# Kernel tuning notes

Hardware: AMD Instinct MI355X
Metric: run time of the kernel (lower is better)

Reference implementation:

```python
import jax, jax.numpy as jnp
import numpy as np

D = 512
H = 8
G = 4          # GroupNorm groups
EPS = 1e-3     # GroupNorm eps


def group_norm(x):
    # x: (b, n, t, d); torch code normalizes per (batch, group) over (n*t, d/G)
    b, n, t, d = x.shape
    xr = x.reshape(b, n * t, G, d // G)
    mu = xr.mean(axis=(1, 3), keepdims=True)
    var = ((xr - mu) ** 2).mean(axis=(1, 3), keepdims=True)
    return ((xr - mu) * jax.lax.rsqrt(var + EPS)).reshape(b, n, t, d)


def setup_inputs() -> dict:
    key = jax.random.key(0)
    ks = jax.random.split(key, 9)
    s = 1.0 / np.sqrt(D)
    inp = {
        "ind": 0,
        "in_f": jax.random.normal(ks[0], (4, 8, 512, D), dtype=jnp.float32),
        "in_f_kv": jax.random.normal(ks[1], (4, 8, 512, D), dtype=jnp.float32),
        "Wq": jax.random.normal(ks[2], (D, D), dtype=jnp.float32) * s,
        "Wk": jax.random.normal(ks[3], (D, D), dtype=jnp.float32) * s,
        "Wv": jax.random.normal(ks[4], (D, D), dtype=jnp.float32) * s,
        "Wz": jax.random.normal(ks[5], (D, D), dtype=jnp.float32) * s,
        "bz": jnp.zeros((D,), dtype=jnp.float32),
        "W1": jax.random.normal(ks[6], (D, D), dtype=jnp.float32) * s,
        "b1": jnp.full((D,), 0.1, dtype=jnp.float32),
        "W2": jax.random.normal(ks[7], (D, D), dtype=jnp.float32) * s,
        "b2": jnp.full((D,), 0.1, dtype=jnp.float32),
    }
    return inp


def reference(ind, in_f, in_f_kv, Wq, Wk, Wv, Wz, bz, W1, b1, W2, b2):
    b, n, t, d = in_f.shape
    hd = d // H
    scale = 1.0 / np.sqrt(hd)

    _in_f = group_norm(in_f)          # LN_1
    _in_f_kv = group_norm(in_f_kv)    # LN_2

    # torch Linear: y = x @ W.T
    q = group_norm(_in_f @ Wq.T)      # LN_3
    k = group_norm(_in_f_kv @ Wk.T)   # LN_4
    v = _in_f_kv @ Wv.T

    q = q.reshape(b, n, t, H, hd)
    k = k.reshape(b, n, -1, H, hd)
    v = v.reshape(b, n, -1, H, hd)

    logits = jnp.einsum('bnqhd,bnkhd->bnhqk', q, k) * scale
    attn_weights = jax.nn.softmax(logits, axis=-1)
    attn_out = jnp.einsum('bnhqk,bnkhd->bnqhd', attn_weights, v).reshape(b, n, t, d)

    in_f_u1 = attn_out @ Wz.T + bz
    in_f_u2 = jax.nn.leaky_relu(_in_f @ W1.T + b1, negative_slope=0.01) @ W2.T + b2

    out_f = in_f + in_f_u1 + in_f_u2
    return (out_f, attn_weights)
```

## Files before the change

### kernel.cpp

```cpp
#include <hip/hip_runtime.h>
#include <math.h>

#define TDIM 512
#define DDIM 512
#define NTROWS 4096
#define MROWS 16384
#define EPSGN 1e-3f

typedef __attribute__((ext_vector_type(8))) short bf16x8;
typedef __attribute__((ext_vector_type(4))) float f32x4;
typedef __attribute__((ext_vector_type(8))) unsigned short us8;
typedef __attribute__((ext_vector_type(4))) unsigned short us4;

__device__ __forceinline__ unsigned short f2b(float f) {
  unsigned int u = __float_as_uint(f);
  return (unsigned short)((u + 0x7fffu + ((u >> 16) & 1u)) >> 16);
}
__device__ __forceinline__ float b2f(unsigned short h) {
  return __uint_as_float(((unsigned int)h) << 16);
}

#define GLOAD16(g, l)                                                                   \
  __builtin_amdgcn_global_load_lds((const __attribute__((address_space(1))) void*)(g),  \
                                   (__attribute__((address_space(3))) void*)(l), 16, 0, 0)

__global__ __launch_bounds__(256) void stats_cvt(const float* __restrict__ x0,
                                                 const float* __restrict__ x1,
                                                 unsigned short* __restrict__ o0,
                                                 unsigned short* __restrict__ o1,
                                                 float* __restrict__ p0,
                                                 float* __restrict__ p1,
                                                 const float* __restrict__ Wz,
                                                 const float* __restrict__ W2,
                                                 unsigned short* __restrict__ w16s) {
  if (blockIdx.y == 2) {
    const int bid = blockIdx.x;
    if (bid >= 256) return;
    const int c = bid * 256 + threadIdx.x;
    const int t = c >> 15;
    const int off = c & 32767;
    const float* s = t ? W2 : Wz;
    unsigned short* d = w16s + (size_t)(16 + t) * 262144;
    const float4 f0 = *(const float4*)(s + (size_t)off * 8);
    const float4 f1 = *(const float4*)(s + (size_t)off * 8 + 4);
    us8 v;
    v[0] = f2b(f0.x); v[1] = f2b(f0.y); v[2] = f2b(f0.z); v[3] = f2b(f0.w);
    v[4] = f2b(f1.x); v[5] = f2b(f1.y); v[6] = f2b(f1.z); v[7] = f2b(f1.w);
    *(us8*)(d + (size_t)off * 8) = v;
    return;
  }
  const float* x = blockIdx.y ? x1 : x0;
  unsigned short* o = blockIdx.y ? o1 : o0;
  float* part = blockIdx.y ? p1 : p0;
  const int blk = blockIdx.x;
  const int batch = blk >> 7;
  const int chunk = blk & 127;
  const size_t base = (size_t)blk * 32 * 512;
  const int tid = threadIdx.x;
  float s = 0.f, sq = 0.f;
#pragma unroll 4
  for (int it = 0; it < 8; ++it) {
    const size_t e = base + (size_t)it * 2048 + (size_t)tid * 8;
    const float4 f0 = *(const float4*)(x + e);
    const float4 f1 = *(const float4*)(x + e + 4);
    us8 v;
    v[0] = f2b(f0.x); v[1] = f2b(f0.y); v[2] = f2b(f0.z); v[3] = f2b(f0.w);
    v[4] = f2b(f1.x); v[5] = f2b(f1.y); v[6] = f2b(f1.z); v[7] = f2b(f1.w);
    *(us8*)(o + e) = v;
    s += f0.x + f0.y + f0.z + f0.w + f1.x + f1.y + f1.z + f1.w;
    sq += f0.x * f0.x + f0.y * f0.y + f0.z * f0.z + f0.w * f0.w +
          f1.x * f1.x + f1.y * f1.y + f1.z * f1.z + f1.w * f1.w;
  }
  const int wave = tid >> 6, lane = tid & 63;
#pragma unroll
  for (int of = 1; of < 16; of <<= 1) { s += __shfl_xor(s, of); sq += __shfl_xor(sq, of); }
  __shared__ float red[4][4][2];
  if ((lane & 15) == 0) { red[wave][lane >> 4][0] = s; red[wave][lane >> 4][1] = sq; }
  __syncthreads();
  if (tid < 4) {
    float S = 0.f, SQ = 0.f;
#pragma unroll
    for (int w = 0; w < 4; ++w) { S += red[w][tid][0]; SQ += red[w][tid][1]; }
    const int idx = (((batch << 2) | tid) << 7) | chunk;
    part[idx * 2] = S;
    part[idx * 2 + 1] = SQ;
  }
}

__global__ __launch_bounds__(256) void wprep(const float* __restrict__ Wq,
                                             const float* __restrict__ Wk,
                                             const float* __restrict__ Wv,
                                             const float* __restrict__ W1,
                                             const float* __restrict__ p0,
                                             const float* __restrict__ p1,
                                             unsigned short* __restrict__ w16s,
                                             float* __restrict__ corr) {
  const int y = blockIdx.y;
  const int w = y >> 2, b = y & 3;
  const float* W = (w == 0) ? Wq : (w == 1) ? Wk : (w == 2) ? Wv : W1;
  const float* part = (w == 0 || w == 3) ? p0 : p1;
  __shared__ float mrs[4][2];
  if (threadIdx.x < 4) {
    const float* p = part + (((b << 2) | threadIdx.x) << 7) * 2;
    float S = 0.f, SQ = 0.f;
    for (int c = 0; c < 128; ++c) { S += p[c * 2]; SQ += p[c * 2 + 1]; }
    const float inv = 1.f / (float)(NTROWS * 128);
    const float mu = S * inv;
    const float var = SQ * inv - mu * mu;
    const float rs = rsqrtf(var + EPSGN);
    mrs[threadIdx.x][0] = rs;
    mrs[threadIdx.x][1] = mu * rs;
  }
  __syncthreads();
  const int wave = threadIdx.x >> 6, lane = threadIdx.x & 63;
  const int n = blockIdx.x * 4 + wave;
  const int k = lane * 8;
  const int g = lane >> 4;
  const float rs = mrs[g][0], murs = mrs[g][1];
  const float4 f0 = *(const float4*)(W + (size_t)n * 512 + k);
  const float4 f1 = *(const float4*)(W + (size_t)n * 512 + k + 4);
  us8 v;
  v[0] = f2b(f0.x * rs); v[1] = f2b(f0.y * rs); v[2] = f2b(f0.z * rs); v[3] = f2b(f0.w * rs);
  v[4] = f2b(f1.x * rs); v[5] = f2b(f1.y * rs); v[6] = f2b(f1.z * rs); v[7] = f2b(f1.w * rs);
  *(us8*)(w16s + (size_t)((w << 2) | b) * 262144 + (size_t)n * 512 + k) = v;
  float t = (f0.x + f0.y + f0.z + f0.w + f1.x + f1.y + f1.z + f1.w) * murs;
#pragma unroll
  for (int of = 1; of < 64; of <<= 1) t += __shfl_xor(t, of);
  if (lane == 0) corr[(((w << 2) | b) << 9) | n] = t;
}

__global__ __launch_bounds__(256) void gemm_all(const unsigned short* __restrict__ a16,
                                                const unsigned short* __restrict__ akv16,
                                                const unsigned short* __restrict__ w16s,
                                                const float* __restrict__ corr,
                                                unsigned short* __restrict__ q16,
                                                unsigned short* __restrict__ h16,
                                                unsigned short* __restrict__ k16,
                                                unsigned short* __restrict__ vTb,
                                                const float* __restrict__ b1,
                                                float* __restrict__ part_q,
                                                float* __restrict__ part_k,
                                                float* __restrict__ sk) {
  __shared__ __align__(16) unsigned short As[128 * 64];
  __shared__ __align__(16) unsigned short Bs[128 * 64];
  __shared__ float red[8];
  const int p = blockIdx.x + (blockIdx.y << 7) + (blockIdx.z << 10);
  const int xc = p & 7, m = p >> 3;
  const int bxi = (xc << 4) | (m & 15);
  const int yi = (m >> 4) & 7;
  const int z = m >> 7;
  const int tid = threadIdx.x;
  const int wave = tid >> 6, lane = tid & 63;
  const int bm = bxi << 7;
  const int batch = bxi >> 5;
  const bool first = yi < 4;
  const int widx = z ? (first ? 1 : 2) : (first ? 0 : 3);
  const unsigned short* A = z ? akv16 : a16;
  const unsigned short* B = w16s + (size_t)262144 * ((widx << 2) | batch);
  const int bnl = (yi & 3) << 7;
  const int wr = (wave >> 1) << 6;
  const int wc = (wave & 1) << 6;
  const int lr = lane & 15, lg = lane >> 4;

  f32x4 acc[4][4] = {};
  const int srow = lane >> 3;
  const int sslot = (lane & 7) ^ srow;

  for (int k0 = 0; k0 < 512; k0 += 64) {
    __syncthreads();
#pragma unroll
    for (int i = 0; i < 4; ++i) {
      const int ci = wave * 4 + i;
      const int row = ci * 8 + srow;
      GLOAD16(A + (size_t)(bm + row) * 512 + k0 + sslot * 8, (char*)As + ci * 1024);
      GLOAD16(B + (size_t)(bnl + row) * 512 + k0 + sslot * 8, (char*)Bs + ci * 1024);
    }
    __syncthreads();
#pragma unroll
    for (int kk = 0; kk < 64; kk += 32) {
      bf16x8 af[4], bfr[4];
#pragma unroll
      for (int i = 0; i < 4; ++i) {
        const int row = wr + i * 16 + lr;
        af[i] = *(const bf16x8*)&As[row * 64 + ((((kk >> 3) + lg) ^ (row & 7)) << 3)];
      }
#pragma unroll
      for (int j = 0; j < 4; ++j) {
        const int row = wc + j * 16 + lr;
        bfr[j] = *(const bf16x8*)&Bs[row * 64 + ((((kk >> 3) + lg) ^ (row & 7)) << 3)];
      }
#pragma unroll
      for (int i = 0; i < 4; ++i)
#pragma unroll
        for (int j = 0; j < 4; ++j)
          acc[i][j] = __builtin_amdgcn_mfma_f32_16x16x32_bf16(af[i], bfr[j], acc[i][j], 0, 0, 0);
    }
  }

  {
    const float* cb = corr + (((widx << 2) | batch) << 9);
    float cj[4];
#pragma unroll
    for (int j = 0; j < 4; ++j) cj[j] = cb[bnl + wc + j * 16 + lr];
#pragma unroll
    for (int i = 0; i < 4; ++i)
#pragma unroll
      for (int j = 0; j < 4; ++j)
#pragma unroll
        for (int r = 0; r < 4; ++r) acc[i][j][r] -= cj[j];
  }

  if (first) {
    unsigned short* C0 = z ? k16 : q16;
#pragma unroll
    for (int i = 0; i < 4; ++i) {
      const int row0 = bm + wr + i * 16 + lg * 4;
#pragma unroll
      for (int j = 0; j < 4; ++j) {
        const int col = bnl + wc + j * 16 + lr;
#pragma unroll
        for (int r = 0; r < 4; ++r)
          C0[(size_t)(row0 + r) * 512 + col] = f2b(acc[i][j][r]);
      }
    }
    float s = 0.f, sq = 0.f;
#pragma unroll
    for (int i = 0; i < 4; ++i)
#pragma unroll
      for (int j = 0; j < 4; ++j)
#pragma unroll
        for (int r = 0; r < 4; ++r) { const float v = acc[i][j][r]; s += v; sq += v * v; }
#pragma unroll
    for (int o = 32; o > 0; o >>= 1) { s += __shfl_xor(s, o); sq += __shfl_xor(sq, o); }
    if (lane == 0) { red[wave * 2] = s; red[wave * 2 + 1] = sq; }
    __syncthreads();
    if (tid == 0) {
      float* part = z ? part_k : part_q;
      const float S = red[0] + red[2] + red[4] + red[6];
      const float SQ = red[1] + red[3] + red[5] + red[7];
      const int slot = bxi & 31, g = yi;
      const int idx = ((((batch << 2) | g) << 5) | slot) << 1;
      part[idx] = S;
      part[idx + 1] = SQ;
    }
    if (z) {
      const int head = (bnl >> 6) + (wave & 1);
#pragma unroll
      for (int i = 0; i < 4; ++i) {
#pragma unroll
        for (int r = 0; r < 4; ++r) {
          float t = acc[i][0][r] + acc[i][1][r] + acc[i][2][r] + acc[i][3][r];
#pragma unroll
          for (int o = 1; o < 16; o <<= 1) t += __shfl_xor(t, o);
          if (lr == 0)
            sk[(size_t)(bm + wr + i * 16 + lg * 4 + r) * 8 + head] = t;
        }
      }
    }
  } else if (z == 0) {
#pragma unroll
    for (int i = 0; i < 4; ++i) {
      const int row0 = bm + wr + i * 16 + lg * 4;
#pragma unroll
      for (int j = 0; j < 4; ++j) {
        const int col = bnl + wc + j * 16 + lr;
        const float bb = b1[col];
#pragma unroll
        for (int r = 0; r < 4; ++r) {
          float v = acc[i][j][r] + bb;
          v = v > 0.f ? v : 0.01f * v;
          h16[(size_t)(row0 + r) * 512 + col] = f2b(v);
        }
      }
    }
  } else {
#pragma unroll
    for (int i = 0; i < 4; ++i) {
      const int row0 = bm + wr + i * 16 + lg * 4;
#pragma unroll
      for (int j = 0; j < 4; ++j) {
        const int col = bnl + wc + j * 16 + lr;
        us4 pk;
#pragma unroll
        for (int r = 0; r < 4; ++r) pk[r] = f2b(acc[i][j][r]);
        *(us4*)&vTb[((size_t)(row0 >> 9) * 512 + col) * 512 + (row0 & 511)] = pk;
      }
    }
  }
}

__global__ __launch_bounds__(256) void gemm_final(const unsigned short* __restrict__ A0,
                                                  const unsigned short* __restrict__ A1,
                                                  const unsigned short* __restrict__ B0,
                                                  const unsigned short* __restrict__ B1,
                                                  float* __restrict__ Cf,
                                                  const float* __restrict__ bias0,
                                                  const float* __restrict__ bias1,
                                                  const unsigned short* __restrict__ init16) {
  __shared__ __align__(16) unsigned short As[128 * 64];
  __shared__ __align__(16) unsigned short Bs[128 * 64];
  const int p = blockIdx.x + (blockIdx.y << 7);
  const int xc = p & 7, m = p >> 3;
  const int bxi = (xc << 4) | (m & 15);
  const int bni = (m >> 4) & 3;
  const int tid = threadIdx.x;
  const int wave = tid >> 6, lane = tid & 63;
  const int bm = bxi << 7, bn = bni << 7;
  const int wr = (wave >> 1) << 6;
  const int wc = (wave & 1) << 6;
  const int lr = lane & 15, lg = lane >> 4;

  f32x4 acc[4][4] = {};
  const int srow = lane >> 3;
  const int sslot = (lane & 7) ^ srow;

  for (int k0 = 0; k0 < 1024; k0 += 64) {
    const unsigned short* Ab = (k0 < 512) ? A0 : A1;
    const unsigned short* Bb = (k0 < 512) ? B0 : B1;
    const int kl = k0 & 511;
    __syncthreads();
#pragma unroll
    for (int i = 0; i < 4; ++i) {
      const int ci = wave * 4 + i;
      const int row = ci * 8 + srow;
      GLOAD16(Ab + (size_t)(bm + row) * 512 + kl + sslot * 8, (char*)As + ci * 1024);
      GLOAD16(Bb + (size_t)(bn + row) * 512 + kl + sslot * 8, (char*)Bs + ci * 1024);
    }
    __syncthreads();
#pragma unroll
    for (int kk = 0; kk < 64; kk += 32) {
      bf16x8 af[4], bfr[4];
#pragma unroll
      for (int i = 0; i < 4; ++i) {
        const int row = wr + i * 16 + lr;
        af[i] = *(const bf16x8*)&As[row * 64 + ((((kk >> 3) + lg) ^ (row & 7)) << 3)];
      }
#pragma unroll
      for (int j = 0; j < 4; ++j) {
        const int row = wc + j * 16 + lr;
        bfr[j] = *(const bf16x8*)&Bs[row * 64 + ((((kk >> 3) + lg) ^ (row & 7)) << 3)];
      }
#pragma unroll
      for (int i = 0; i < 4; ++i)
#pragma unroll
        for (int j = 0; j < 4; ++j)
          acc[i][j] = __builtin_amdgcn_mfma_f32_16x16x32_bf16(af[i], bfr[j], acc[i][j], 0, 0, 0);
    }
  }

#pragma unroll
  for (int i = 0; i < 4; ++i) {
    const int row0 = bm + wr + i * 16 + lg * 4;
#pragma unroll
    for (int j = 0; j < 4; ++j) {
      const int col = bn + wc + j * 16 + lr;
      const float bb = bias0[col] + bias1[col];
#pragma unroll
      for (int r = 0; r < 4; ++r) {
        const size_t o = (size_t)(row0 + r) * 512 + col;
        Cf[o] = acc[i][j][r] + bb + b2f(init16[o]);
      }
    }
  }
}

__global__ __launch_bounds__(256) void attn_fused(const unsigned short* __restrict__ q16,
                                                  const unsigned short* __restrict__ k16,
                                                  const unsigned short* __restrict__ vT,
                                                  const float* __restrict__ part_q,
                                                  const float* __restrict__ part_k,
                                                  const float* __restrict__ sk,
                                                  float* __restrict__ aw,
                                                  unsigned short* __restrict__ ao16) {
  __shared__ __align__(16) char smem[73728];
  unsigned short* Qs = (unsigned short*)smem;
  unsigned short* Ks = (unsigned short*)(smem + 8192);
  unsigned short* Ps = (unsigned short*)(smem + 40960);
  float* Pf = (float*)smem;
  __shared__ float WM[4][64];
  __shared__ float WS[4][64];
  __shared__ float sk_lds[512];
  __shared__ float cst[2];

  const int p = blockIdx.x;
  const int xcd = p & 7, seq = p >> 3;
  const int bid = (xcd << 5) | (seq >> 3);
  const int q0 = (seq & 7) << 6;
  const int h = bid & 7;
  const int b = bid >> 6;
  const int tid = threadIdx.x;
  const int w = tid >> 6, lane = tid & 63;
  const int lr = lane & 15, lg = lane >> 4;
  const int srow = lane >> 3;
  const int sslot = (lane & 7) ^ srow;

  const size_t hb = (size_t)(bid >> 3) * (512 * 512);
  const unsigned short* Qg = q16 + hb + h * 64;
  const unsigned short* Kg = k16 + hb + h * 64;
  const unsigned short* Vg = vT + hb + (size_t)h * 64 * 512;

  if (tid == 0) {
    const int pbase = (((b << 2) | (h >> 1)) << 6);
    const float* pq = part_q + pbase;
    const float* pk = part_k + pbase;
    float Sq = 0.f, SQq = 0.f, Sk = 0.f, SQk = 0.f;
    for (int c = 0; c < 32; ++c) {
      Sq += pq[c * 2]; SQq += pq[c * 2 + 1];
      Sk += pk[c * 2]; SQk += pk[c * 2 + 1];
    }
    const float inv = 1.f / (float)(NTROWS * 128);
    const float muq = Sq * inv, vq = SQq * inv - muq * muq;
    const float muk = Sk * inv, vk = SQk * inv - muk * muk;
    const float a = rsqrtf(vq + EPSGN) * rsqrtf(vk + EPSGN) * 0.125f;
    cst[0] = a;
    cst[1] = a * muq;
  }
  {
    const float* skg = sk + (size_t)(bid >> 3) * 512 * 8 + h;
    for (int j = tid; j < 512; j += 256) sk_lds[j] = skg[(size_t)j * 8];
  }

#pragma unroll
  for (int it = 0; it < 2; ++it) {
    const int ci = w * 2 + it;
    const int row = ci * 8 + srow;
    GLOAD16(Qg + (size_t)(q0 + row) * 512 + sslot * 8, (char*)Qs + ci * 1024);
  }

  f32x4 sc[4][8] = {};

#pragma unroll
  for (int half = 0; half < 2; ++half) {
    __syncthreads();
#pragma unroll
    for (int it = 0; it < 8; ++it) {
      const int ci = w * 8 + it;
      const int row = ci * 8 + srow;
      GLOAD16(Kg + (size_t)(half * 256 + row) * 512 + sslot * 8, (char*)Ks + ci * 1024);
    }
    __syncthreads();
#pragma unroll
    for (int kk = 0; kk < 64; kk += 32) {
      bf16x8 aq[4];
#pragma unroll
      for (int qf = 0; qf < 4; ++qf) {
        const int row = qf * 16 + lr;
        aq[qf] = *(const bf16x8*)&Qs[row * 64 + ((((kk >> 3) + lg) ^ (row & 7)) << 3)];
      }
#pragma unroll
      for (int kf = 0; kf < 4; ++kf) {
        const int row = w * 64 + kf * 16 + lr;
        const bf16x8 bk = *(const bf16x8*)&Ks[row * 64 + ((((kk >> 3) + lg) ^ (row & 7)) << 3)];
#pragma unroll
        for (int qf = 0; qf < 4; ++qf)
          sc[qf][half * 4 + kf] =
              __builtin_amdgcn_mfma_f32_16x16x32_bf16(aq[qf], bk, sc[qf][half * 4 + kf], 0, 0, 0);
      }
    }
  }

  const float aSc = cst[0], cmu = cst[1];
#pragma unroll
  for (int qf = 0; qf < 4; ++qf)
#pragma unroll
    for (int kfi = 0; kfi < 8; ++kfi) {
      const int k = ((kfi >> 2) << 8) + w * 64 + ((kfi & 3) << 4) + lr;
      const float corr = cmu * sk_lds[k];
#pragma unroll
      for (int r = 0; r < 4; ++r) sc[qf][kfi][r] = aSc * sc[qf][kfi][r] - corr;
    }

  float Mv[4][4];
#pragma unroll
  for (int qf = 0; qf < 4; ++qf)
#pragma unroll
    for (int r = 0; r < 4; ++r) {
      float m = sc[qf][0][r];
#pragma unroll
      for (int kf = 1; kf < 8; ++kf) m = fmaxf(m, sc[qf][kf][r]);
#pragma unroll
      for (int o = 1; o < 16; o <<= 1) m = fmaxf(m, __shfl_xor(m, o));
      Mv[qf][r] = m;
    }
  if (lr == 0) {
#pragma unroll
    for (int qf = 0; qf < 4; ++qf)
#pragma unroll
      for (int r = 0; r < 4; ++r) WM[w][qf * 16 + lg * 4 + r] = Mv[qf][r];
  }
  __syncthreads();
#pragma unroll
  for (int qf = 0; qf < 4; ++qf)
#pragma unroll
    for (int r = 0; r < 4; ++r) {
      const int q = qf * 16 + lg * 4 + r;
      Mv[qf][r] = fmaxf(fmaxf(WM[0][q], WM[1][q]), fmaxf(WM[2][q], WM[3][q]));
    }
  float sl[4][4] = {};
#pragma unroll
  for (int qf = 0; qf < 4; ++qf)
#pragma unroll
    for (int kf = 0; kf < 8; ++kf) {
      f32x4 v = sc[qf][kf];
#pragma unroll
      for (int r = 0; r < 4; ++r) {
        const float e = __expf(v[r] - Mv[qf][r]);
        v[r] = e;
        sl[qf][r] += e;
      }
      sc[qf][kf] = v;
    }
#pragma unroll
  for (int qf = 0; qf < 4; ++qf)
#pragma unroll
    for (int r = 0; r < 4; ++r) {
      float s = sl[qf][r];
#pragma unroll
      for (int o = 1; o < 16; o <<= 1) s += __shfl_xor(s, o);
      sl[qf][r] = s;
    }
  if (lr == 0) {
#pragma unroll
    for (int qf = 0; qf < 4; ++qf)
#pragma unroll
      for (int r = 0; r < 4; ++r) WS[w][qf * 16 + lg * 4 + r] = sl[qf][r];
  }
  __syncthreads();
#pragma unroll
  for (int qf = 0; qf < 4; ++qf)
#pragma unroll
    for (int r = 0; r < 4; ++r) {
      const int q = qf * 16 + lg * 4 + r;
      const float inv = 1.f / (WS[0][q] + WS[1][q] + WS[2][q] + WS[3][q]);
#pragma unroll
      for (int kf = 0; kf < 8; ++kf) sc[qf][kf][r] *= inv;
    }

  float* AWp = aw + ((size_t)bid * 512 + q0) * 512;
#pragma unroll
  for (int half = 0; half < 2; ++half) {
#pragma unroll
    for (int qf = 0; qf < 4; ++qf)
#pragma unroll
      for (int s2 = 0; s2 < 4; ++s2) {
        const int kl = w * 64 + (s2 << 4) + lr;
#pragma unroll
        for (int r = 0; r < 4; ++r) {
          const int q = qf * 16 + lg * 4 + r;
          Pf[q * 260 + kl] = sc[qf][half * 4 + s2][r];
        }
      }
    __syncthreads();
#pragma unroll
    for (int rr = 0; rr < 16; ++rr) {
      const int q = w * 16 + rr;
      const f32x4 v = *(const f32x4*)&Pf[q * 260 + lane * 4];
      __builtin_nontemporal_store(
          v, (f32x4*)&AWp[(size_t)q * 512 + half * 256 + lane * 4]);
    }
    __syncthreads();
  }

#pragma unroll
  for (int it = 0; it < 8; ++it) {
    const int ci = w * 8 + it;
    const int row = ci * 2 + (lane >> 5);
    const int s = lane & 31;
    GLOAD16(Vg + (size_t)row * 512 + ((s ^ (row & 7)) << 3), (char*)Ks + ci * 1024);
  }
#pragma unroll
  for (int qf = 0; qf < 4; ++qf)
#pragma unroll
    for (int r = 0; r < 4; ++r) {
      const int q = qf * 16 + lg * 4 + r;
#pragma unroll
      for (int kf = 0; kf < 4; ++kf) {
        const int k = w * 64 + (kf << 4) + lr;
        Ps[q * 256 + (((k >> 3) ^ (q & 7)) << 3) + (k & 7)] = f2b(sc[qf][kf][r]);
      }
    }
  __syncthreads();

  f32x4 accO[4] = {};
#pragma unroll
  for (int ks = 0; ks < 256; ks += 32) {
    const int sl0 = ks >> 3;
    const int q = w * 16 + lr;
    const bf16x8 af = *(const bf16x8*)&Ps[q * 256 + (((sl0 + lg) ^ (q & 7)) << 3)];
#pragma unroll
    for (int df = 0; df < 4; ++df) {
      const int row = df * 16 + lr;
      const bf16x8 vb = *(const bf16x8*)&Ks[row * 256 + (((sl0 + lg) ^ (row & 7)) << 3)];
      accO[df] = __builtin_amdgcn_mfma_f32_16x16x32_bf16(af, vb, accO[df], 0, 0, 0);
    }
  }
  __syncthreads();

#pragma unroll
  for (int it = 0; it < 8; ++it) {
    const int ci = w * 8 + it;
    const int row = ci * 2 + (lane >> 5);
    const int s = lane & 31;
    GLOAD16(Vg + (size_t)row * 512 + 256 + ((s ^ (row & 7)) << 3), (char*)Ks + ci * 1024);
  }
#pragma unroll
  for (int qf = 0; qf < 4; ++qf)
#pragma unroll
    for (int r = 0; r < 4; ++r) {
      const int q = qf * 16 + lg * 4 + r;
#pragma unroll
      for (int kf = 0; kf < 4; ++kf) {
        const int k = w * 64 + (kf << 4) + lr;
        Ps[q * 256 + (((k >> 3) ^ (q & 7)) << 3) + (k & 7)] = f2b(sc[qf][4 + kf][r]);
      }
    }
  __syncthreads();

#pragma unroll
  for (int ks = 0; ks < 256; ks += 32) {
    const int sl0 = ks >> 3;
    const int q = w * 16 + lr;
    const bf16x8 af = *(const bf16x8*)&Ps[q * 256 + (((sl0 + lg) ^ (q & 7)) << 3)];
#pragma unroll
    for (int df = 0; df < 4; ++df) {
      const int row = df * 16 + lr;
      const bf16x8 vb = *(const bf16x8*)&Ks[row * 256 + (((sl0 + lg) ^ (row & 7)) << 3)];
      accO[df] = __builtin_amdgcn_mfma_f32_16x16x32_bf16(af, vb, accO[df], 0, 0, 0);
    }
  }

  const int growb = (bid >> 3) * 512 + q0 + w * 16 + lg * 4;
#pragma unroll
  for (int df = 0; df < 4; ++df)
#pragma unroll
    for (int r = 0; r < 4; ++r)
      ao16[(size_t)(growb + r) * 512 + h * 64 + df * 16 + lr] = f2b(accO[df][r]);
}

extern "C" void kernel_launch(void* const* d_in, const int* in_sizes, int n_in,
                              void* d_out, int out_size, void* d_ws, size_t ws_size,
                              hipStream_t stream) {
  const float* in_f = (const float*)d_in[1];
  const float* in_fkv = (const float*)d_in[2];
  const float* Wq = (const float*)d_in[3];
  const float* Wk = (const float*)d_in[4];
  const float* Wv = (const float*)d_in[5];
  const float* Wz = (const float*)d_in[6];
  const float* bz = (const float*)d_in[7];
  const float* W1 = (const float*)d_in[8];
  const float* b1 = (const float*)d_in[9];
  const float* W2 = (const float*)d_in[10];
  const float* b2 = (const float*)d_in[11];

  float* out_f = (float*)d_out;
  float* attw = out_f + (size_t)MROWS * DDIM;

  const size_t TSB = (size_t)MROWS * DDIM;
  unsigned short* us = (unsigned short*)d_ws;
  unsigned short* a16 = us;
  unsigned short* akv16 = us + TSB;
  unsigned short* q16 = us + 2 * TSB;
  unsigned short* k16 = us + 3 * TSB;
  unsigned short* h16 = us + 4 * TSB;
  unsigned short* ao16 = us + 5 * TSB;
  unsigned short* vT = us + 6 * TSB;
  unsigned short* w16s = us + 7 * TSB;
  float* fbase = (float*)(us + 7 * TSB + 18 * 262144);
  float* p0 = fbase;
  float* p1 = fbase + 4096;
  float* part_q = fbase + 8192;
  float* part_k = fbase + 9216;
  float* corr = fbase + 10240;
  float* sk = fbase + 18432;

  stats_cvt<<<dim3(512, 3), 256, 0, stream>>>(in_f, in_fkv, a16, akv16, p0, p1, Wz, W2, w16s);
  wprep<<<dim3(128, 16), 256, 0, stream>>>(Wq, Wk, Wv, W1, p0, p1, w16s, corr);
  gemm_all<<<dim3(128, 8, 2), 256, 0, stream>>>(a16, akv16, w16s, corr, q16, h16, k16, vT, b1,
                                                part_q, part_k, sk);
  attn_fused<<<2048, 256, 0, stream>>>(q16, k16, vT, part_q, part_k, sk, attw, ao16);
  gemm_final<<<dim3(128, 4), 256, 0, stream>>>(ao16, h16, w16s + 16 * 262144,
                                               w16s + 17 * 262144, out_f, bz, b2, a16);
}
```

Before: 230.2 us.

## Prefetch first V half during softmax and attention-weight writeback by reorganizing LDS

Reassigns LDS regions so the first half of V is loaded into a separate buffer right after QK^T, overlapping its global load with the softmax and attention-weight store. The fp32 staging for attention-weight writeback is shrunk to 128-column chunks over four passes so it no longer overlaps the V buffer. P is now staged in the former K region. The cost is more barriers and passes in the writeback, with only half the waves writing each chunk.

```diff
diff --git a/kernel.cpp b/kernel.cpp
--- a/kernel.cpp
+++ b/kernel.cpp
@@ -374,8 +374,8 @@
                                                   unsigned short* __restrict__ ao16) {
   __shared__ __align__(16) char smem[73728];
   unsigned short* Qs = (unsigned short*)smem;
-  unsigned short* Ks = (unsigned short*)(smem + 8192);
-  unsigned short* Ps = (unsigned short*)(smem + 40960);
+  unsigned short* KsP = (unsigned short*)(smem + 8192);
+  unsigned short* PsV = (unsigned short*)(smem + 40960);
   float* Pf = (float*)smem;
   __shared__ float WM[4][64];
   __shared__ float WS[4][64];
@@ -436,7 +436,7 @@
     for (int it = 0; it < 8; ++it) {
       const int ci = w * 8 + it;
       const int row = ci * 8 + srow;
-      GLOAD16(Kg + (size_t)(half * 256 + row) * 512 + sslot * 8, (char*)Ks + ci * 1024);
+      GLOAD16(Kg + (size_t)(half * 256 + row) * 512 + sslot * 8, (char*)KsP + ci * 1024);
     }
     __syncthreads();
 #pragma unroll
@@ -450,13 +450,21 @@
 #pragma unroll
       for (int kf = 0; kf < 4; ++kf) {
         const int row = w * 64 + kf * 16 + lr;
-        const bf16x8 bk = *(const bf16x8*)&Ks[row * 64 + ((((kk >> 3) + lg) ^ (row & 7)) << 3)];
+        const bf16x8 bk = *(const bf16x8*)&KsP[row * 64 + ((((kk >> 3) + lg) ^ (row & 7)) << 3)];
 #pragma unroll
         for (int qf = 0; qf < 4; ++qf)
           sc[qf][half * 4 + kf] =
               __builtin_amdgcn_mfma_f32_16x16x32_bf16(aq[qf], bk, sc[qf][half * 4 + kf], 0, 0, 0);
       }
     }
+  }
+
+#pragma unroll
+  for (int it = 0; it < 8; ++it) {
+    const int ci = w * 8 + it;
+    const int row = ci * 2 + (lane >> 5);
+    const int s = lane & 31;
+    GLOAD16(Vg + (size_t)row * 512 + ((s ^ (row & 7)) << 3), (char*)PsV + ci * 1024);
   }
 
   const float aSc = cst[0], cmu = cst[1];
@@ -538,35 +546,68 @@
 
   float* AWp = aw + ((size_t)bid * 512 + q0) * 512;
 #pragma unroll
-  for (int half = 0; half < 2; ++half) {
-#pragma unroll
-    for (int qf = 0; qf < 4; ++qf)
-#pragma unroll
-      for (int s2 = 0; s2 < 4; ++s2) {
-        const int kl = w * 64 + (s2 << 4) + lr;
-#pragma unroll
-        for (int r = 0; r < 4; ++r) {
-          const int q = qf * 16 + lg * 4 + r;
-          Pf[q * 260 + kl] = sc[qf][half * 4 + s2][r];
+  for (int c = 0; c < 4; ++c) {
+    const int half = c >> 1;
+    if ((w >> 1) == (c & 1)) {
+      const int base_kl = (w & 1) << 6;
+#pragma unroll
+      for (int qf = 0; qf < 4; ++qf)
+#pragma unroll
+        for (int s2 = 0; s2 < 4; ++s2) {
+          const int kl = base_kl + (s2 << 4) + lr;
+#pragma unroll
+          for (int r = 0; r < 4; ++r) {
+            const int q = qf * 16 + lg * 4 + r;
+            Pf[q * 136 + kl] = sc[qf][half * 4 + s2][r];
+          }
         }
-      }
-    __syncthreads();
-#pragma unroll
-    for (int rr = 0; rr < 16; ++rr) {
-      const int q = w * 16 + rr;
-      const f32x4 v = *(const f32x4*)&Pf[q * 260 + lane * 4];
+    }
+    __syncthreads();
+#pragma unroll
+    for (int rr = 0; rr < 8; ++rr) {
+      const int q = w * 16 + rr * 2 + (lane >> 5);
+      const int col = (lane & 31) * 4;
+      const f32x4 v = *(const f32x4*)&Pf[q * 136 + col];
       __builtin_nontemporal_store(
-          v, (f32x4*)&AWp[(size_t)q * 512 + half * 256 + lane * 4]);
-    }
-    __syncthreads();
-  }
+          v, (f32x4*)&AWp[(size_t)q * 512 + c * 128 + col]);
+    }
+    __syncthreads();
+  }
+
+#pragma unroll
+  for (int qf = 0; qf < 4; ++qf)
+#pragma unroll
+    for (int r = 0; r < 4; ++r) {
+      const int q = qf * 16 + lg * 4 + r;
+#pragma unroll
+      for (int kf = 0; kf < 4; ++kf) {
+        const int k = w * 64 + (kf << 4) + lr;
+        KsP[q * 256 + (((k >> 3) ^ (q & 7)) << 3) + (k & 7)] = f2b(sc[qf][kf][r]);
+      }
+    }
+  __syncthreads();
+
+  f32x4 accO[4] = {};
+#pragma unroll
+  for (int ks = 0; ks < 256; ks += 32) {
+    const int sl0 = ks >> 3;
+    const int q = w * 16 + lr;
+    const bf16x8 af = *(const bf16x8*)&KsP[q * 256 + (((sl0 + lg) ^ (q & 7)) << 3)];
+#pragma unroll
+    for (int df = 0; df < 4; ++df) {
+      const int row = df * 16 + lr;
+      const bf16x8 vb = *(const bf16x8*)&PsV[row * 256 + (((sl0 + lg) ^ (row & 7)) << 3)];
+      accO[df] = __builtin_amdgcn_mfma_f32_16x16x32_bf16(af, vb, accO[df], 0, 0, 0);
+    }
+  }
+  __syncthreads();
 
 #pragma unroll
   for (int it = 0; it < 8; ++it) {
     const int ci = w * 8 + it;
     const int row = ci * 2 + (lane >> 5);
     const int s = lane & 31;
-    GLOAD16(Vg + (size_t)row * 512 + ((s ^ (row & 7)) << 3), (char*)Ks + ci * 1024);
+    GLOAD16(Vg + (size_t)row * 512 + 256 + ((s ^ (row & 7)) << 3), (char*)PsV + ci * 1024);
   }
 #pragma unroll
   for (int qf = 0; qf < 4; ++qf)
@@ -576,55 +617,20 @@
 #pragma unroll
       for (int kf = 0; kf < 4; ++kf) {
         const int k = w * 64 + (kf << 4) + lr;
-        Ps[q * 256 + (((k >> 3) ^ (q & 7)) << 3) + (k & 7)] = f2b(sc[qf][kf][r]);
+        KsP[q * 256 + (((k >> 3) ^ (q & 7)) << 3) + (k & 7)] = f2b(sc[qf][4 + kf][r]);
       }
     }
   __syncthreads();
 
-  f32x4 accO[4] = {};
 #pragma unroll
   for (int ks = 0; ks < 256; ks += 32) {
     const int sl0 = ks >> 3;
     const int q = w * 16 + lr;
-    const bf16x8 af = *(const bf16x8*)&Ps[q * 256 + (((sl0 + lg) ^ (q & 7)) << 3)];
+    const bf16x8 af = *(const bf16x8*)&KsP[q * 256 + (((sl0 + lg) ^ (q & 7)) << 3)];
 #pragma unroll
     for (int df = 0; df < 4; ++df) {
       const int row = df * 16 + lr;
-      const bf16x8 vb = *(const bf16x8*)&Ks[row * 256 + (((sl0 + lg) ^ (row & 7)) << 3)];
-      accO[df] = __builtin_amdgcn_mfma_f32_16x16x32_bf16(af, vb, accO[df], 0, 0, 0);
-    }
-  }
-  __syncthreads();
-
-#pragma unroll
-  for (int it = 0; it < 8; ++it) {
-    const int ci = w * 8 + it;
-    const int row = ci * 2 + (lane >> 5);
-    const int s = lane & 31;
-    GLOAD16(Vg + (size_t)row * 512 + 256 + ((s ^ (row & 7)) << 3), (char*)Ks + ci * 1024);
-  }
-#pragma unroll
-  for (int qf = 0; qf < 4; ++qf)
-#pragma unroll
-    for (int r = 0; r < 4; ++r) {
-      const int q = qf * 16 + lg * 4 + r;
-#pragma unroll
-      for (int kf = 0; kf < 4; ++kf) {
-        const int k = w * 64 + (kf << 4) + lr;
-        Ps[q * 256 + (((k >> 3) ^ (q & 7)) << 3) + (k & 7)] = f2b(sc[qf][4 + kf][r]);
-      }
-    }
-  __syncthreads();
-
-#pragma unroll
-  for (int ks = 0; ks < 256; ks += 32) {
-    const int sl0 = ks >> 3;
-    const int q = w * 16 + lr;
-    const bf16x8 af = *(const bf16x8*)&Ps[q * 256 + (((sl0 + lg) ^ (q & 7)) << 3)];
-#pragma unroll
-    for (int df = 0; df < 4; ++df) {
-      const int row = df * 16 + lr;
-      const bf16x8 vb = *(const bf16x8*)&Ks[row * 256 + (((sl0 + lg) ^ (row & 7)) << 3)];
+      const bf16x8 vb = *(const bf16x8*)&PsV[row * 256 + (((sl0 + lg) ^ (row & 7)) << 3)];
       accO[df] = __builtin_amdgcn_mfma_f32_16x16x32_bf16(af, vb, accO[df], 0, 0, 0);
     }
   }
```

Result: no change. 230.0 us (-0.0%).
